# Kernel tuning notes

Hardware: AMD Instinct MI355X
Metric: run time of the kernel (lower is better)

Reference implementation:

```python
import jax, jax.numpy as jnp
import numpy as np

D = 1024

def setup_inputs() -> dict:
    key = jax.random.key(0)
    kx, kw = jax.random.split(key)
    x = jax.random.normal(kx, (4, 2048, D), dtype=jnp.float32)
    # nn.Linear(d, 3d, bias=False): weight [3d, d]; y = x @ W.T
    W = jax.random.normal(kw, (3 * D, D), dtype=jnp.float32) * (1.0 / np.sqrt(D))
    return {"x": x, "W": W}

def reference(x, W):
    d = x.shape[-1]
    qkv = jnp.einsum('bsd,ed->bse', x, W)  # [B,S,3d]
    q, k, v = jnp.split(qkv, 3, axis=2)
    att = jnp.einsum('bqd,bkd->bqk', q, k) * (1.0 / jnp.sqrt(jnp.asarray(d, x.dtype)))
    att = jax.nn.softmax(att, axis=-1)
    y = jnp.einsum('bqk,bkd->bqd', att, v)
    return y
```

## Files before the change

### kernel.cpp

```cpp
#include <hip/hip_runtime.h>
#include <hip/hip_bf16.h>


typedef __attribute__((ext_vector_type(8))) short short8;
typedef __attribute__((ext_vector_type(4))) float f32x4;

typedef unsigned short u16;

__device__ __forceinline__ u16 f32_to_bf16(float f) {
    unsigned int u = __float_as_uint(f);
    u += 0x7fffu + ((u >> 16) & 1u);
    return (u16)(u >> 16);
}

__device__ __forceinline__ void gload16(const u16* g, u16* lds_base) {
    __builtin_amdgcn_global_load_lds(
        (const __attribute__((address_space(1))) void*)g,
        (__attribute__((address_space(3))) void*)lds_base, 16, 0, 0);
}

__device__ __forceinline__ void bar() { __builtin_amdgcn_s_barrier(); }
__device__ __forceinline__ void bar_end() {
    __builtin_amdgcn_sched_barrier(0);
    __builtin_amdgcn_s_barrier();
}
__device__ __forceinline__ void wait_vm8() {
    asm volatile("s_waitcnt vmcnt(8)" ::: "memory");
}
__device__ __forceinline__ void wait_vm7() {
    asm volatile("s_waitcnt vmcnt(7)" ::: "memory");
}
__device__ __forceinline__ void wait_vm6() {
    asm volatile("s_waitcnt vmcnt(6)" ::: "memory");
}
__device__ __forceinline__ void wait_vm3() {
    asm volatile("s_waitcnt vmcnt(3)" ::: "memory");
}
__device__ __forceinline__ void wait_vm2() {
    asm volatile("s_waitcnt vmcnt(2)" ::: "memory");
}
__device__ __forceinline__ void wait_vm0() {
    asm volatile("s_waitcnt vmcnt(0)" ::: "memory");
}

__global__ void cast_inputs(const float* __restrict__ x, u16* __restrict__ Xb,
                            const float* __restrict__ W, u16* __restrict__ Wb,
                            float* __restrict__ l,
                            int nx4, int nw4, int nl) {
    int i = blockIdx.x * blockDim.x + threadIdx.x;
    if (i >= nx4 + nw4) {
        int idx = i - (nx4 + nw4);
        if (idx < nl) l[idx] = 0.f;
        return;
    }
    const float* in; u16* out; int idx;
    if (i < nx4) { in = x; out = Xb; idx = i; }
    else { idx = i - nx4; in = W; out = Wb; }
    float4 v = ((const float4*)in)[idx];
    ushort4 o;
    o.x = f32_to_bf16(v.x); o.y = f32_to_bf16(v.y);
    o.z = f32_to_bf16(v.z); o.w = f32_to_bf16(v.w);
    ((ushort4*)out)[idx] = o;
}


struct Acc256 { f32x4 acc[8][4]; };
struct Acc192 { f32x4 acc[8][3]; };
struct Acc128 { f32x4 acc[8][2]; };

template<int MH>
__device__ __forceinline__ void rd_a(const u16* __restrict__ sA, int wr, int lane,
                                     int lr, short8 (&af)[4][2]) {
#pragma unroll
    for (int a2 = 0; a2 < 4; ++a2) {
        const int row = wr * 128 + MH * 64 + a2 * 16 + lr;
#pragma unroll
        for (int k2 = 0; k2 < 2; ++k2) {
            const int cb = (lane >> 4) + k2 * 4;
            af[a2][k2] = *(const short8*)(sA + row * 64 + ((cb ^ (lr & 7)) * 8));
        }
    }
}

template<int NH>
__device__ __forceinline__ void rd_b(const u16* __restrict__ sB, int wc, int lane,
                                     int lr, short8 (&bf)[2][2]) {
#pragma unroll
    for (int b2 = 0; b2 < 2; ++b2) {
        const int row = wc * 64 + NH * 32 + b2 * 16 + lr;
#pragma unroll
        for (int k2 = 0; k2 < 2; ++k2) {
            const int cb = (lane >> 4) + k2 * 4;
            bf[b2][k2] = *(const short8*)(sB + row * 64 + ((cb ^ (lr & 7)) * 8));
        }
    }
}

template<int MH, int NH>
__device__ __forceinline__ void mm_q(Acc256& fr, const short8 (&af)[4][2],
                                     const short8 (&bf)[2][2]) {
    __builtin_amdgcn_s_setprio(1);
#pragma unroll
    for (int a2 = 0; a2 < 4; ++a2)
#pragma unroll
        for (int b2 = 0; b2 < 2; ++b2)
#pragma unroll
            for (int k2 = 0; k2 < 2; ++k2)
                fr.acc[MH * 4 + a2][NH * 2 + b2] =
                    __builtin_amdgcn_mfma_f32_16x16x32_bf16(
                        af[a2][k2], bf[b2][k2],
                        fr.acc[MH * 4 + a2][NH * 2 + b2], 0, 0, 0);
    __builtin_amdgcn_s_setprio(0);
}

__device__ __forceinline__ void rd_b01(const u16* __restrict__ sB, int wc, int lane,
                                       int lr, short8 (&bf)[2][2]) {
#pragma unroll
    for (int b2 = 0; b2 < 2; ++b2) {
        const int row = wc * 48 + b2 * 16 + lr;
#pragma unroll
        for (int k2 = 0; k2 < 2; ++k2) {
            const int cb = (lane >> 4) + k2 * 4;
            bf[b2][k2] = *(const short8*)(sB + row * 64 + ((cb ^ (lr & 7)) * 8));
        }
    }
}

__device__ __forceinline__ void rd_b2(const u16* __restrict__ sB, int wc, int lane,
                                      int lr, short8 (&bf)[2]) {
    const int row = wc * 48 + 32 + lr;
#pragma unroll
    for (int k2 = 0; k2 < 2; ++k2) {
        const int cb = (lane >> 4) + k2 * 4;
        bf[k2] = *(const short8*)(sB + row * 64 + ((cb ^ (lr & 7)) * 8));
    }
}

template<int MH>
__device__ __forceinline__ void mm_b01(Acc192& fr, const short8 (&af)[4][2],
                                       const short8 (&bf)[2][2]) {
    __builtin_amdgcn_s_setprio(1);
#pragma unroll
    for (int a2 = 0; a2 < 4; ++a2)
#pragma unroll
        for (int b2 = 0; b2 < 2; ++b2)
#pragma unroll
            for (int k2 = 0; k2 < 2; ++k2)
                fr.acc[MH * 4 + a2][b2] =
                    __builtin_amdgcn_mfma_f32_16x16x32_bf16(
                        af[a2][k2], bf[b2][k2],
                        fr.acc[MH * 4 + a2][b2], 0, 0, 0);
    __builtin_amdgcn_s_setprio(0);
}

template<int MH>
__device__ __forceinline__ void mm_b2(Acc192& fr, const short8 (&af)[4][2],
                                      const short8 (&bf)[2]) {
    __builtin_amdgcn_s_setprio(1);
#pragma unroll
    for (int a2 = 0; a2 < 4; ++a2)
#pragma unroll
        for (int k2 = 0; k2 < 2; ++k2)
            fr.acc[MH * 4 + a2][2] =
                __builtin_amdgcn_mfma_f32_16x16x32_bf16(
                    af[a2][k2], bf[k2], fr.acc[MH * 4 + a2][2], 0, 0, 0);
    __builtin_amdgcn_s_setprio(0);
}

template<int BI>
__device__ __forceinline__ void rd_b1f(const u16* __restrict__ sB, int wc, int lane,
                                       int lr, short8 (&bf)[2]) {
    const int row = wc * 32 + BI * 16 + lr;
#pragma unroll
    for (int k2 = 0; k2 < 2; ++k2) {
        const int cb = (lane >> 4) + k2 * 4;
        bf[k2] = *(const short8*)(sB + row * 64 + ((cb ^ (lr & 7)) * 8));
    }
}

template<int MH, int BI>
__device__ __forceinline__ void mm_h(Acc128& fr, const short8 (&af)[4][2],
                                     const short8 (&bf)[2]) {
    __builtin_amdgcn_s_setprio(1);
#pragma unroll
    for (int a2 = 0; a2 < 4; ++a2)
#pragma unroll
        for (int k2 = 0; k2 < 2; ++k2)
            fr.acc[MH * 4 + a2][BI] =
                __builtin_amdgcn_mfma_f32_16x16x32_bf16(
                    af[a2][k2], bf[k2], fr.acc[MH * 4 + a2][BI], 0, 0, 0);
    __builtin_amdgcn_s_setprio(0);
}

__device__ __forceinline__ void gemm_core_256(
    const u16* __restrict__ A, const u16* __restrict__ Bt,
    int K, int lda, int ldb, int row0, int col0, u16* sm, Acc256& fr)
{
    const int t    = threadIdx.x;
    const int lane = t & 63;
    const int wave = t >> 6;
    const int wr   = wave >> 2;
    const int wc   = wave & 3;
    const int lr   = lane & 15;
    const int srow = lane >> 3;
    const int gc   = (lane & 7) ^ srow;

    const u16* const sA0 = sm;
    const u16* const sA1 = sm + 16384;
    const u16* const sB0 = sm + 32768;
    const u16* const sB1 = sm + 49152;

#pragma unroll
    for (int a = 0; a < 8; ++a)
#pragma unroll
        for (int b = 0; b < 4; ++b)
            fr.acc[a][b] = (f32x4){0.f, 0.f, 0.f, 0.f};

    const u16* aB = A  + (long long)(row0 + wave * 8 + srow) * lda + gc * 8;
    const u16* bB = Bt + (long long)(col0 + wave * 8 + srow) * ldb + gc * 8;
    u16* const sAw = sm + wave * 512;
    u16* const sBw = sm + 32768 + wave * 512;

    auto stageA = [&](int kt) {
        u16* d = sAw + (kt & 1) * 16384;
        const u16* g = aB + kt * 64;
#pragma unroll
        for (int r4 = 0; r4 < 4; ++r4)
            gload16(g + (long long)(r4 * 64) * lda, d + r4 * 4096);
    };
    auto stageB = [&](int kt) {
        u16* d = sBw + (kt & 1) * 16384;
        const u16* g = bB + kt * 64;
#pragma unroll
        for (int r4 = 0; r4 < 4; ++r4)
            gload16(g + (long long)(r4 * 64) * ldb, d + r4 * 4096);
    };

    stageA(0); stageB(0); stageA(1); stageB(1);
    wait_vm8();
    bar();

    const int NI = K >> 7;
    short8 af[4][2], bfa[2][2], bfb[2][2];
#pragma unroll 1
    for (int i = 0; i < NI; ++i) {
        const bool more = (i + 1 < NI);
        const int t2 = 2 * i + 2;

        rd_a<0>(sA0, wr, lane, lr, af);
        rd_b<0>(sB0, wc, lane, lr, bfa);
        bar();
        mm_q<0, 0>(fr, af, bfa);
        bar_end();

        rd_b<1>(sB0, wc, lane, lr, bfb);
        bar();
        mm_q<0, 1>(fr, af, bfb);
        bar_end();

        rd_a<1>(sA0, wr, lane, lr, af);
        if (more) stageB(t2);
        bar();
        mm_q<1, 1>(fr, af, bfb);
        bar_end();

        if (more) stageA(t2);
        bar();
        mm_q<1, 0>(fr, af, bfa);
        if (more) wait_vm8(); else wait_vm0();
        bar_end();

        rd_a<0>(sA1, wr, lane, lr, af);
        rd_b<0>(sB1, wc, lane, lr, bfa);
        bar();
        mm_q<0, 0>(fr, af, bfa);
        bar_end();

        rd_b<1>(sB1, wc, lane, lr, bfb);
        bar();
        mm_q<0, 1>(fr, af, bfb);
        bar_end();

        rd_a<1>(sA1, wr, lane, lr, af);
        if (more) stageB(t2 + 1);
        bar();
        mm_q<1, 1>(fr, af, bfb);
        bar_end();

        if (more) stageA(t2 + 1);
        bar();
        mm_q<1, 0>(fr, af, bfa);
        if (more) wait_vm8();
        bar_end();
    }
}

__device__ __forceinline__ void gemm_core_192(
    const u16* __restrict__ A, const u16* __restrict__ Bt,
    int K, int lda, int ldb, int row0, int col0, u16* sm, Acc192& fr)
{
    const int t    = threadIdx.x;
    const int lane = t & 63;
    const int wave = t >> 6;
    const int wr   = wave >> 2;
    const int wc   = wave & 3;
    const int lr   = lane & 15;
    const int srow = lane >> 3;
    const int gc   = (lane & 7) ^ srow;

    const u16* const sA0 = sm;
    const u16* const sA1 = sm + 16384;
    const u16* const sB0 = sm + 32768;
    const u16* const sB1 = sm + 45056;

#pragma unroll
    for (int a = 0; a < 8; ++a)
#pragma unroll
        for (int b = 0; b < 3; ++b)
            fr.acc[a][b] = (f32x4){0.f, 0.f, 0.f, 0.f};

    const u16* aB = A  + (long long)(row0 + wave * 8 + srow) * lda + gc * 8;
    const u16* bB = Bt + (long long)(col0 + wave * 8 + srow) * ldb + gc * 8;
    u16* const sAw = sm + wave * 512;
    u16* const sBw = sm + 32768 + wave * 512;

    auto stageA = [&](int kt) {
        u16* d = sAw + (kt & 1) * 16384;
        const u16* g = aB + kt * 64;
#pragma unroll
        for (int r4 = 0; r4 < 4; ++r4)
            gload16(g + (long long)(r4 * 64) * lda, d + r4 * 4096);
    };
    auto stageB = [&](int kt) {
        u16* d = sBw + (kt & 1) * 12288;
        const u16* g = bB + kt * 64;
#pragma unroll
        for (int r4 = 0; r4 < 3; ++r4)
            gload16(g + (long long)(r4 * 64) * ldb, d + r4 * 4096);
    };

    stageA(0); stageB(0); stageA(1); stageB(1);
    wait_vm7();
    bar();

    short8 afP[4][2], afQ[4][2], bfaP[2][2], bfaQ[2][2], bfb[2];
    rd_a<0>(sA0, wr, lane, lr, afP);
    rd_b01(sB0, wc, lane, lr, bfaP);

    const int NT = K >> 6;
#pragma unroll 1
    for (int i = 0; i < NT; i += 2) {
        const bool more = (i + 2 < NT);

        rd_b2(sB0, wc, lane, lr, bfb);
        mm_b01<0>(fr, afP, bfaP);
        bar();

        rd_a<1>(sA0, wr, lane, lr, afQ);
        mm_b2<0>(fr, afP, bfb);
        bar();

        mm_b2<1>(fr, afQ, bfb);
        __builtin_amdgcn_sched_barrier(0);
        if (more) { stageB(i + 2); wait_vm3(); } else wait_vm0();
        bar();

        rd_a<0>(sA1, wr, lane, lr, afP);
        rd_b01(sB1, wc, lane, lr, bfaQ);
        mm_b01<1>(fr, afQ, bfaP);
        __builtin_amdgcn_sched_barrier(0);
        if (more) stageA(i + 2);
        bar();

        rd_b2(sB1, wc, lane, lr, bfb);
        mm_b01<0>(fr, afP, bfaQ);
        bar();

        rd_a<1>(sA1, wr, lane, lr, afQ);
        mm_b2<0>(fr, afP, bfb);
        bar();

        mm_b2<1>(fr, afQ, bfb);
        __builtin_amdgcn_sched_barrier(0);
        if (more) { stageB(i + 3); wait_vm3(); } else wait_vm0();
        bar();

        if (more) {
            rd_a<0>(sA0, wr, lane, lr, afP);
            rd_b01(sB0, wc, lane, lr, bfaP);
        }
        mm_b01<1>(fr, afQ, bfaQ);
        __builtin_amdgcn_sched_barrier(0);
        if (more) stageA(i + 3);
        bar();
    }
}

__device__ __forceinline__ void gemm_core_n128(
    const u16* __restrict__ A, const u16* __restrict__ Bt,
    int K, int lda, int ldb, int row0, int col0, u16* sm, Acc128& fr)
{
    const int t    = threadIdx.x;
    const int lane = t & 63;
    const int wave = t >> 6;
    const int wr   = wave >> 2;
    const int wc   = wave & 3;
    const int lr   = lane & 15;
    const int srow = lane >> 3;
    const int gc   = (lane & 7) ^ srow;

    const u16* const sA0 = sm;
    const u16* const sA1 = sm + 16384;
    const u16* const sB0 = sm + 32768;
    const u16* const sB1 = sm + 40960;

#pragma unroll
    for (int a = 0; a < 8; ++a)
#pragma unroll
        for (int b = 0; b < 2; ++b)
            fr.acc[a][b] = (f32x4){0.f, 0.f, 0.f, 0.f};

    const u16* aB = A  + (long long)(row0 + wave * 8 + srow) * lda + gc * 8;
    const u16* bB = Bt + (long long)(col0 + wave * 8 + srow) * ldb + gc * 8;
    u16* const sAw = sm + wave * 512;
    u16* const sBw = sm + 32768 + wave * 512;

    auto stageA = [&](int kt) {
        u16* d = sAw + (kt & 1) * 16384;
        const u16* g = aB + kt * 64;
#pragma unroll
        for (int r4 = 0; r4 < 4; ++r4)
            gload16(g + (long long)(r4 * 64) * lda, d + r4 * 4096);
    };
    auto stageB = [&](int kt) {
        u16* d = sBw + (kt & 1) * 8192;
        const u16* g = bB + kt * 64;
#pragma unroll
        for (int r4 = 0; r4 < 2; ++r4)
            gload16(g + (long long)(r4 * 64) * ldb, d + r4 * 4096);
    };

    stageB(0); stageA(0); stageB(1); stageA(1);
    wait_vm6();
    bar();

    short8 afP[4][2], afQ[4][2], b0P[2], b0Q[2], bfb[2];
    rd_a<0>(sA0, wr, lane, lr, afP);
    rd_b1f<0>(sB0, wc, lane, lr, b0P);

    const int NT = K >> 6;
#pragma unroll 1
    for (int i = 0; i < NT; i += 2) {
        const bool more = (i + 2 < NT);

        rd_b1f<1>(sB0, wc, lane, lr, bfb);
        mm_h<0, 0>(fr, afP, b0P);
        bar();

        rd_a<1>(sA0, wr, lane, lr, afQ);
        mm_h<0, 1>(fr, afP, bfb);
        bar();

        mm_h<1, 1>(fr, afQ, bfb);
        __builtin_amdgcn_sched_barrier(0);
        if (more) { stageB(i + 2); wait_vm2(); } else wait_vm0();
        bar();

        rd_a<0>(sA1, wr, lane, lr, afP);
        rd_b1f<0>(sB1, wc, lane, lr, b0Q);
        mm_h<1, 0>(fr, afQ, b0P);
        __builtin_amdgcn_sched_barrier(0);
        if (more) stageA(i + 2);
        bar();

        rd_b1f<1>(sB1, wc, lane, lr, bfb);
        mm_h<0, 0>(fr, afP, b0Q);
        bar();

        rd_a<1>(sA1, wr, lane, lr, afQ);
        mm_h<0, 1>(fr, afP, bfb);
        bar();

        mm_h<1, 1>(fr, afQ, bfb);
        __builtin_amdgcn_sched_barrier(0);
        if (more) { stageB(i + 3); wait_vm2(); } else wait_vm0();
        bar();

        if (more) {
            rd_a<0>(sA0, wr, lane, lr, afP);
            rd_b1f<0>(sB0, wc, lane, lr, b0P);
        }
        mm_h<1, 0>(fr, afQ, b0Q);
        __builtin_amdgcn_sched_barrier(0);
        if (more) stageA(i + 3);
        bar();
    }
}


__global__ __launch_bounds__(512, 1) void gemm_qkv(
    const u16* __restrict__ Xb, const u16* __restrict__ Wb,
    u16* __restrict__ QK, u16* __restrict__ VT)
{
    __shared__ u16 sm[57344];
    const int row0 = blockIdx.y * 256;
    const int col0 = blockIdx.x * 192;

    Acc192 fr;
    gemm_core_192(Xb, Wb, 1024, 1024, 1024, row0, col0, sm, fr);

    const int lane = threadIdx.x & 63;
    const int wave = threadIdx.x >> 6;
    const int wr = wave >> 2, wc = wave & 3;
    const int cr = (lane >> 4) * 4, cc = lane & 15;

#pragma unroll
    for (int a = 0; a < 8; ++a) {
        const int grow = row0 + wr * 128 + a * 16 + cr;
#pragma unroll
        for (int b = 0; b < 3; ++b) {
            const int gcol = col0 + wc * 48 + b * 16 + cc;
            if (gcol < 2048) {
#pragma unroll
                for (int r = 0; r < 4; ++r)
                    QK[(long long)(grow + r) * 2048 + gcol] =
                        f32_to_bf16(fr.acc[a][b][r]);
            } else {
                const int bz = grow >> 11, s = grow & 2047;
                const int d = gcol - 2048;
                ushort4 o;
                o.x = f32_to_bf16(fr.acc[a][b][0]);
                o.y = f32_to_bf16(fr.acc[a][b][1]);
                o.z = f32_to_bf16(fr.acc[a][b][2]);
                o.w = f32_to_bf16(fr.acc[a][b][3]);
                *(ushort4*)(&VT[((long long)(bz * 1024 + d)) * 2048 + s]) = o;
            }
        }
    }
}

__global__ __launch_bounds__(512, 1) void gemm_s_exp(
    const u16* __restrict__ QK, u16* __restrict__ E, float* __restrict__ l)
{
    __shared__ u16 sm[65536];
    const long long boff = (long long)blockIdx.z * 2048 * 2048;
    const u16* Q  = QK + boff;
    const u16* Kp = QK + boff + 1024;
    u16* Eb = E + boff;
    float* lb = l + (long long)blockIdx.z * 2048;
    const int row0 = blockIdx.y * 256;
    const int col0 = blockIdx.x * 256;

    Acc256 fr;
    gemm_core_256(Q, Kp, 1024, 2048, 2048, row0, col0, sm, fr);

    const int lane = threadIdx.x & 63;
    const int wave = threadIdx.x >> 6;
    const int wr = wave >> 2, wc = wave & 3;
    const int cr = (lane >> 4) * 4, cc = lane & 15;

#pragma unroll
    for (int a = 0; a < 8; ++a) {
        float rs[4] = {0.f, 0.f, 0.f, 0.f};
#pragma unroll
        for (int b = 0; b < 4; ++b)
#pragma unroll
            for (int r = 0; r < 4; ++r) {
                float e = __expf(fr.acc[a][b][r] * 0.03125f);
                rs[r] += e;
                int grow = row0 + wr * 128 + a * 16 + cr + r;
                int gcol = col0 + wc * 64 + b * 16 + cc;
                Eb[(long long)grow * 2048 + gcol] = f32_to_bf16(e);
            }
#pragma unroll
        for (int r = 0; r < 4; ++r) {
#pragma unroll
            for (int m = 1; m < 16; m <<= 1) rs[r] += __shfl_xor(rs[r], m, 64);
            if ((lane & 15) == 0)
                atomicAdd(&lb[row0 + wr * 128 + a * 16 + cr + r], rs[r]);
        }
    }
}

__global__ __launch_bounds__(512, 1) void gemm_pv(
    const u16* __restrict__ E, const u16* __restrict__ VT,
    const float* __restrict__ l, float* __restrict__ Y)
{
    __shared__ u16 sm[49152];
    const int lin = blockIdx.x + 8 * (blockIdx.y + 8 * blockIdx.z);
    const int wid = (lin & 7) * 32 + (lin >> 3);
    const int dy = wid & 7;
    const int qx = (wid >> 3) & 7;
    const int bz = wid >> 6;

    const u16* Eb  = E  + (long long)bz * 2048 * 2048;
    const u16* VTb = VT + (long long)bz * 1024 * 2048;
    const float* lb = l + (long long)bz * 2048;
    float* Yb = Y + (long long)bz * 2048 * 1024;
    const int row0 = qx * 256;
    const int col0 = dy * 128;

    Acc128 fr;
    gemm_core_n128(Eb, VTb, 2048, 2048, 2048, row0, col0, sm, fr);

    const int lane = threadIdx.x & 63;
    const int wave = threadIdx.x >> 6;
    const int wr = wave >> 2, wc = wave & 3;
    const int cr = (lane >> 4) * 4, cc = lane & 15;

#pragma unroll
    for (int a = 0; a < 8; ++a) {
        const int q0 = row0 + wr * 128 + a * 16 + cr;
        const float4 l4 = *(const float4*)(&lb[q0]);
        const float inv0 = 1.0f / l4.x, inv1 = 1.0f / l4.y;
        const float inv2 = 1.0f / l4.z, inv3 = 1.0f / l4.w;
#pragma unroll
        for (int b = 0; b < 2; ++b) {
            const int d = col0 + wc * 32 + b * 16 + cc;
            Yb[(long long)(q0 + 0) * 1024 + d] = fr.acc[a][b][0] * inv0;
            Yb[(long long)(q0 + 1) * 1024 + d] = fr.acc[a][b][1] * inv1;
            Yb[(long long)(q0 + 2) * 1024 + d] = fr.acc[a][b][2] * inv2;
            Yb[(long long)(q0 + 3) * 1024 + d] = fr.acc[a][b][3] * inv3;
        }
    }
}

extern "C" void kernel_launch(void* const* d_in, const int* in_sizes, int n_in,
                              void* d_out, int out_size, void* d_ws, size_t ws_size,
                              hipStream_t stream) {
    const float* x = (const float*)d_in[0];
    const float* W = (const float*)d_in[1];
    float* out = (float*)d_out;

    char* ws = (char*)d_ws;
    u16*   Xb = (u16*)(ws);
    u16*   Wb = (u16*)(ws + 16777216LL);
    u16*   QK = (u16*)(ws + 23068672LL);
    u16*   VT = (u16*)(ws + 56623104LL);
    u16*   E  = (u16*)(ws + 73400320LL);
    float* l  = (float*)(ws + 106954752LL);

    const int nx4 = 8192 * 1024 / 4, nw4 = 3072 * 1024 / 4;
    cast_inputs<<<11296, 256, 0, stream>>>(x, Xb, W, Wb, l, nx4, nw4, 8192);
    gemm_qkv<<<dim3(16, 32, 1), 512, 0, stream>>>(Xb, Wb, QK, VT);
    gemm_s_exp<<<dim3(8, 8, 4), 512, 0, stream>>>(QK, E, l);
    gemm_pv<<<dim3(8, 8, 4), 512, 0, stream>>>(E, VT, l, out);
}
```

Measured before the change: 219.9 us.

## Software-pipeline LDS fragment reads with MFMA in GEMM main loop

Restructures the GEMM k-loop so that LDS fragment reads for the next quarter-step are issued alongside the current MFMA block. Two A-fragment register sets are used, and the first fragments of the following tile are prefetched before the loop ends. Global-to-LDS staging is reordered (B earlier, A after the last reads) with a vmcnt(4) wait, and several barriers are dropped. The goal is to hide LDS read latency behind matrix math, at the cost of higher register pressure and tighter LDS hazard ordering.

```diff
diff --git a/kernel.cpp b/kernel.cpp
--- a/kernel.cpp
+++ b/kernel.cpp
@@ -32,6 +32,9 @@
 }
 __device__ __forceinline__ void wait_vm6() {
     asm volatile("s_waitcnt vmcnt(6)" ::: "memory");
+}
+__device__ __forceinline__ void wait_vm4() {
+    asm volatile("s_waitcnt vmcnt(4)" ::: "memory");
 }
 __device__ __forceinline__ void wait_vm3() {
     asm volatile("s_waitcnt vmcnt(3)" ::: "memory");
@@ -240,58 +243,56 @@
     wait_vm8();
     bar();
 
-    const int NI = K >> 7;
-    short8 af[4][2], bfa[2][2], bfb[2][2];
+    short8 afP[4][2], afQ[4][2], bfa[2][2], bfb[2][2];
+    rd_a<0>(sA0, wr, lane, lr, afP);
+    rd_b<0>(sB0, wc, lane, lr, bfa);
+
+    const int NT = K >> 6;
 #pragma unroll 1
-    for (int i = 0; i < NI; ++i) {
-        const bool more = (i + 1 < NI);
-        const int t2 = 2 * i + 2;
-
-        rd_a<0>(sA0, wr, lane, lr, af);
-        rd_b<0>(sB0, wc, lane, lr, bfa);
-        bar();
-        mm_q<0, 0>(fr, af, bfa);
-        bar_end();
+    for (int i = 0; i < NT; i += 2) {
+        const bool more = (i + 2 < NT);
 
         rd_b<1>(sB0, wc, lane, lr, bfb);
-        bar();
-        mm_q<0, 1>(fr, af, bfb);
-        bar_end();
-
-        rd_a<1>(sA0, wr, lane, lr, af);
-        if (more) stageB(t2);
-        bar();
-        mm_q<1, 1>(fr, af, bfb);
-        bar_end();
-
-        if (more) stageA(t2);
-        bar();
-        mm_q<1, 0>(fr, af, bfa);
-        if (more) wait_vm8(); else wait_vm0();
-        bar_end();
-
-        rd_a<0>(sA1, wr, lane, lr, af);
+        mm_q<0, 0>(fr, afP, bfa);
+        bar();
+
+        rd_a<1>(sA0, wr, lane, lr, afQ);
+        mm_q<0, 1>(fr, afP, bfb);
+        bar();
+
+        mm_q<1, 0>(fr, afQ, bfa);
+        __builtin_amdgcn_sched_barrier(0);
+        if (more) { stageB(i + 2); wait_vm4(); } else wait_vm0();
+        bar();
+
+        rd_a<0>(sA1, wr, lane, lr, afP);
         rd_b<0>(sB1, wc, lane, lr, bfa);
-        bar();
-        mm_q<0, 0>(fr, af, bfa);
-        bar_end();
+        mm_q<1, 1>(fr, afQ, bfb);
+        __builtin_amdgcn_sched_barrier(0);
+        if (more) stageA(i + 2);
+        bar();
 
         rd_b<1>(sB1, wc, lane, lr, bfb);
-        bar();
-        mm_q<0, 1>(fr, af, bfb);
-        bar_end();
-
-        rd_a<1>(sA1, wr, lane, lr, af);
-        if (more) stageB(t2 + 1);
-        bar();
-        mm_q<1, 1>(fr, af, bfb);
-        bar_end();
-
-        if (more) stageA(t2 + 1);
-        bar();
-        mm_q<1, 0>(fr, af, bfa);
-        if (more) wait_vm8();
-        bar_end();
+        mm_q<0, 0>(fr, afP, bfa);
+        bar();
+
+        rd_a<1>(sA1, wr, lane, lr, afQ);
+        mm_q<0, 1>(fr, afP, bfb);
+        bar();
+
+        mm_q<1, 0>(fr, afQ, bfa);
+        __builtin_amdgcn_sched_barrier(0);
+        if (more) { stageB(i + 3); wait_vm4(); } else wait_vm0();
+        bar();
+
+        if (more) {
+            rd_a<0>(sA0, wr, lane, lr, afP);
+            rd_b<0>(sB0, wc, lane, lr, bfa);
+        }
+        mm_q<1, 1>(fr, afQ, bfb);
+        __builtin_amdgcn_sched_barrier(0);
+        if (more) stageA(i + 3);
+        bar();
     }
 }
 
```

New measurement: 224.3 us. No clear change (+2.0%).
